# Kernel tuning notes

Hardware: AMD Instinct MI355X
Metric: run time of the kernel (lower is better)

## Reference

```python
import jax, jax.numpy as jnp
import numpy as np

N_NODES = 100000
N_EDGES = 1600000
IN_DIM = 128
EMB = 64
HID = 2 * EMB  # 128


def gcn_conv(x, W, b, row, col, norm):
    # PyG GCNConv: h = x @ W, then aggregate norm-weighted messages src->dst, then +bias
    h = x @ W                                   # [N, out]
    msg = norm[:, None] * h[row]                # gather over source nodes [E', out]
    out = jax.ops.segment_sum(msg, col, num_segments=N_NODES)  # scatter to targets
    return out + b


def gcn_norm(edge_index, edge_weight, n_nodes):
    # add self-loops with weight 1, then symmetric normalization D^-1/2 A D^-1/2
    loop = jnp.arange(n_nodes, dtype=edge_index.dtype)
    row = jnp.concatenate([edge_index[0], loop])
    col = jnp.concatenate([edge_index[1], loop])
    ew = jnp.concatenate([edge_weight, jnp.ones((n_nodes,), edge_weight.dtype)])
    deg = jax.ops.segment_sum(ew, col, num_segments=n_nodes)
    dinv = jnp.where(deg > 0, jax.lax.rsqrt(deg), 0.0)
    norm = dinv[row] * ew * dinv[col]
    return row, col, norm


def setup_inputs() -> dict:
    key = jax.random.key(0)
    ks = jax.random.split(key, 10)
    x = jax.random.normal(ks[0], (N_NODES, IN_DIM), dtype=jnp.float32)
    edge_index = jax.random.randint(ks[1], (2, N_EDGES), 0, N_NODES, dtype=jnp.int64)
    edge_weight = jax.random.uniform(ks[2], (N_EDGES,), dtype=jnp.float32)
    s1 = 1.0 / np.sqrt(IN_DIM)
    s2 = 1.0 / np.sqrt(HID)
    W1 = jax.random.uniform(ks[3], (IN_DIM, HID), jnp.float32, -s1, s1)
    b1 = jnp.zeros((HID,), jnp.float32)
    Wmu = jax.random.uniform(ks[4], (HID, EMB), jnp.float32, -s2, s2)
    bmu = jnp.zeros((EMB,), jnp.float32)
    Wlv = jax.random.uniform(ks[5], (HID, EMB), jnp.float32, -s2, s2)
    blv = jnp.zeros((EMB,), jnp.float32)
    return {"x": x, "edge_index": edge_index, "edge_weight": edge_weight,
            "W1": W1, "b1": b1, "Wmu": Wmu, "bmu": bmu, "Wlv": Wlv, "blv": blv}


def reference(x, edge_index, edge_weight, W1, b1, Wmu, bmu, Wlv, blv):
    row, col, norm = gcn_norm(edge_index, edge_weight, N_NODES)
    h = jax.nn.relu(gcn_conv(x, W1, b1, row, col, norm))
    mu = gcn_conv(h, Wmu, bmu, row, col, norm)
    logvar = gcn_conv(h, Wlv, blv, row, col, norm)
    return (mu, logvar)
```

## Files before the change

kernel.cpp:

```cpp
#include <hip/hip_runtime.h>

#define NN 100000
#define NE 1600000
#define DD 128
#define OUT_HALF 6400000
#define CAP 64

#define NB 256
#define NPB 391
#define BCAP 8192
#define BSTRIDE 64
#define CHUNK 6144
#define CPT 24

#define GNM 64
#define XPITCH 140

typedef unsigned int uint_t;
typedef float v4f __attribute__((ext_vector_type(4)));
typedef short v8s __attribute__((ext_vector_type(8)));

__device__ __forceinline__ unsigned short f2bf(float f) {
    uint_t u = __float_as_uint(f);
    u = (u + 0x7fffu + ((u >> 16) & 1u)) >> 16;
    return (unsigned short)u;
}
__device__ __forceinline__ float bf2f(unsigned short h) {
    return __uint_as_float(((uint_t)h) << 16);
}
__device__ __forceinline__ float bf_lo(uint_t u) { return __uint_as_float(u << 16); }
__device__ __forceinline__ float bf_hi(uint_t u) { return __uint_as_float(u & 0xffff0000u); }

#define EW_SCALE 32767.0f
#define EW_INV (1.0f / 32767.0f)


__global__ void k_zero(int* __restrict__ bcnt) {
    int i = blockIdx.x * blockDim.x + threadIdx.x;
    if (i < NB * BSTRIDE) bcnt[i] = 0;
}

__launch_bounds__(256)
__global__ void k_bin(const int* __restrict__ row, const int* __restrict__ col,
                      const float* __restrict__ ew, int* __restrict__ bcnt,
                      uint2* __restrict__ bins) {
    __shared__ uint2 sorted[CHUNK];
    __shared__ int hist[NB];
    __shared__ int lstart[NB];
    __shared__ int offs[NB];
    __shared__ int gbase[NB];
    const int tid = threadIdx.x;
    const int ebase = blockIdx.x * CHUNK;
    const int nloc = (NE - ebase < CHUNK) ? (NE - ebase) : CHUNK;

    hist[tid] = 0;
    __syncthreads();

    for (int k = 0; k < CPT; ++k) {
        int i = ebase + k * 256 + tid;
        if (i < NE) {
            uint_t b = (uint_t)col[i] / NPB;
            atomicAdd(&hist[b], 1);
        }
    }
    __syncthreads();

    int v = hist[tid];
#pragma unroll
    for (int s = 1; s < NB; s <<= 1) {
        int t = (tid >= s) ? hist[tid - s] : 0;
        __syncthreads();
        hist[tid] += t;
        __syncthreads();
    }
    int excl = hist[tid] - v;
    lstart[tid] = excl;
    offs[tid] = excl;
    gbase[tid] = atomicAdd(&bcnt[tid * BSTRIDE], v);
    __syncthreads();

    for (int k = 0; k < CPT; ++k) {
        int i = ebase + k * 256 + tid;
        if (i < NE) {
            uint_t c = (uint_t)col[i];
            uint_t r = (uint_t)row[i];
            uint_t q = (uint_t)__float2int_rn(ew[i] * EW_SCALE);
            uint_t b = c / NPB;
            int pos = atomicAdd(&offs[b], 1);
            sorted[pos] = make_uint2((r << 15) | q, c);
        }
    }
    __syncthreads();

    for (int i = tid; i < nloc; i += 256) {
        uint2 rec = sorted[i];
        uint_t b = rec.y / NPB;
        int dst = gbase[b] + (i - lstart[b]);
        if (dst < BCAP) bins[(size_t)b * BCAP + dst] = rec;
    }
}

__launch_bounds__(512)
__global__ void k_scatter(const int* __restrict__ bcnt, const uint2* __restrict__ bins,
                          int* __restrict__ cnt, uint_t* __restrict__ slots,
                          float* __restrict__ dinv) {
    __shared__ int combo[NPB];
    const int b = blockIdx.x;
    const int tid = threadIdx.x;
    if (tid < NPB) combo[tid] = 0;
    __syncthreads();
    int n = bcnt[b * BSTRIDE];
    n = (n < BCAP) ? n : BCAP;
    const int base = b * NPB;
    const uint2* seg = bins + (size_t)b * BCAP;
    for (int i = tid; i < n; i += 512) {
        uint2 rec = seg[i];
        int lc = (int)rec.y - base;
        uint_t w = rec.x & 0x7fffu;
        uint_t old = (uint_t)atomicAdd(&combo[lc], (int)((1u << 22) | w));
        uint_t pos = old >> 22;
        if (pos < CAP) slots[rec.y * CAP + pos] = rec.x;
    }
    __syncthreads();
    if (tid < NPB) {
        int node = base + tid;
        if (node < NN) {
            uint_t v = (uint_t)combo[tid];
            int c = (int)(v >> 22);
            cnt[node] = (c < CAP) ? c : CAP;
            dinv[node] = rsqrtf(1.0f + (float)(v & 0x3fffffu) * EW_INV);
        }
    }
}


template <bool RELU, bool OUT_BF16>
__launch_bounds__(256)
__global__ void k_gather(const uint_t* __restrict__ src, const int* __restrict__ cnt,
                         const uint_t* __restrict__ slots, const float* __restrict__ dinv,
                         const float* __restrict__ bias, void* __restrict__ dst) {
    int wid = (blockIdx.x * blockDim.x + threadIdx.x) >> 6;
    int lane = threadIdx.x & 63;
    if (wid >= NN) return;
    float di = dinv[wid];
    uint_t u = src[wid * 64 + lane];
    float accx = bf_lo(u);
    float accy = bf_hi(u);
    int end = __builtin_amdgcn_readfirstlane(cnt[wid]);
    const uint_t* seg = slots + wid * CAP;
    for (int jj = 0; jj < end; jj += 8) {
        uint_t rp[8];
#pragma unroll
        for (int q = 0; q < 8; ++q) {
            int idx = (jj + q < end) ? (jj + q) : (end - 1);
            rp[q] = seg[idx];
        }
        uint_t sv[8];
#pragma unroll
        for (int q = 0; q < 8; ++q) {
            sv[q] = src[(rp[q] >> 15) * 64 + lane];
        }
#pragma unroll
        for (int q = 0; q < 8; ++q) {
            float p = (jj + q < end) ? (float)(rp[q] & 0x7fffu) * EW_INV : 0.0f;
            accx = fmaf(p, bf_lo(sv[q]), accx);
            accy = fmaf(p, bf_hi(sv[q]), accy);
        }
    }
    accx *= di;
    accy *= di;
    if (RELU) {
        float2 b = ((const float2*)bias)[lane];
        accx = fmaxf(accx + b.x, 0.0f) * di;
        accy = fmaxf(accy + b.y, 0.0f) * di;
    }
    if (OUT_BF16) {
        ((uint_t*)dst)[wid * 64 + lane] =
            (uint_t)f2bf(accx) | ((uint_t)f2bf(accy) << 16);
    } else {
        ((float2*)dst)[wid * 64 + lane] = make_float2(accx, accy);
    }
}


__launch_bounds__(256)
__global__ void k_gemm_h0(const float* __restrict__ X, const float* __restrict__ W,
                          const float* __restrict__ dinv,
                          unsigned short* __restrict__ Y) {
    __shared__ float xs[GNM * XPITCH];
    const int tid = threadIdx.x;
    const int node0 = blockIdx.x * GNM;

    {
        const float4* X4 = (const float4*)X;
        for (int i = tid; i < GNM * 32; i += 256) {
            int row = i >> 5, kg = i & 31;
            int ne = node0 + row;
            if (ne >= NN) ne = NN - 1;
            *(float4*)&xs[row * XPITCH + kg * 4] = X4[ne * 32 + kg];
        }
    }
    __syncthreads();

    const int wave = tid >> 6, lane = tid & 63;
    const int la = lane >> 4, ln = lane & 15;
    const float* xrow = &xs[(wave * 16 + ln) * XPITCH];

    v4f acc[8];
#pragma unroll
    for (int nt = 0; nt < 8; ++nt) acc[nt] = (v4f){0.f, 0.f, 0.f, 0.f};

    for (int kt = 0; kt < 4; ++kt) {
        float4 xa0 = *(const float4*)&xrow[kt * 32 + la * 4];
        float4 xa1 = *(const float4*)&xrow[kt * 32 + la * 4 + 16];
        float xv[8] = {xa0.x, xa0.y, xa0.z, xa0.w, xa1.x, xa1.y, xa1.z, xa1.w};
        v8s ah, al;
#pragma unroll
        for (int j = 0; j < 8; ++j) {
            unsigned short h = f2bf(xv[j]);
            ah[j] = (short)h;
            al[j] = (short)f2bf(xv[j] - bf2f(h));
        }
        const float* Wb = W + (kt * 32 + la * 4) * 128 + ln;
#pragma unroll
        for (int nt = 0; nt < 8; ++nt) {
            v8s bh;
#pragma unroll
            for (int j4 = 0; j4 < 4; ++j4) {
                bh[j4] = (short)f2bf(Wb[j4 * 128 + nt * 16]);
                bh[j4 + 4] = (short)f2bf(Wb[(j4 + 16) * 128 + nt * 16]);
            }
            acc[nt] = __builtin_amdgcn_mfma_f32_16x16x32_bf16(ah, bh, acc[nt], 0, 0, 0);
            acc[nt] = __builtin_amdgcn_mfma_f32_16x16x32_bf16(al, bh, acc[nt], 0, 0, 0);
        }
    }

#pragma unroll
    for (int r = 0; r < 4; ++r) {
        int node = node0 + wave * 16 + la * 4 + r;
        if (node < NN) {
            float di = dinv[node];
#pragma unroll
            for (int nt = 0; nt < 8; ++nt)
                Y[node * 128 + nt * 16 + ln] = f2bf(acc[nt][r] * di);
        }
    }
}

__launch_bounds__(256)
__global__ void k_gemm_out(const float* __restrict__ G, const float* __restrict__ Wmu,
                           const float* __restrict__ Wlv, const float* __restrict__ bmu,
                           const float* __restrict__ blv, float* __restrict__ out) {
    __shared__ float xs[GNM * XPITCH];
    const int tid = threadIdx.x;
    const int node0 = blockIdx.x * GNM;

    {
        const float4* G4 = (const float4*)G;
        for (int i = tid; i < GNM * 32; i += 256) {
            int row = i >> 5, kg = i & 31;
            int ne = node0 + row;
            if (ne >= NN) ne = NN - 1;
            *(float4*)&xs[row * XPITCH + kg * 4] = G4[ne * 32 + kg];
        }
    }
    __syncthreads();

    const int wave = tid >> 6, lane = tid & 63;
    const int la = lane >> 4, ln = lane & 15;
    const float* xrow = &xs[(wave * 16 + ln) * XPITCH];

    v4f acc[8];
#pragma unroll
    for (int nt = 0; nt < 8; ++nt) acc[nt] = (v4f){0.f, 0.f, 0.f, 0.f};

    for (int kt = 0; kt < 4; ++kt) {
        float4 xa0 = *(const float4*)&xrow[kt * 32 + la * 4];
        float4 xa1 = *(const float4*)&xrow[kt * 32 + la * 4 + 16];
        float xv[8] = {xa0.x, xa0.y, xa0.z, xa0.w, xa1.x, xa1.y, xa1.z, xa1.w};
        v8s ah, al;
#pragma unroll
        for (int j = 0; j < 8; ++j) {
            unsigned short h = f2bf(xv[j]);
            ah[j] = (short)h;
            al[j] = (short)f2bf(xv[j] - bf2f(h));
        }
        const float* Wmb = Wmu + (kt * 32 + la * 4) * 64 + ln;
        const float* Wlb = Wlv + (kt * 32 + la * 4) * 64 + ln;
#pragma unroll
        for (int nt = 0; nt < 8; ++nt) {
            const float* Wb = (nt < 4) ? Wmb : Wlb;
            const int co = (nt & 3) * 16;
            v8s bh;
#pragma unroll
            for (int j4 = 0; j4 < 4; ++j4) {
                bh[j4] = (short)f2bf(Wb[j4 * 64 + co]);
                bh[j4 + 4] = (short)f2bf(Wb[(j4 + 16) * 64 + co]);
            }
            acc[nt] = __builtin_amdgcn_mfma_f32_16x16x32_bf16(ah, bh, acc[nt], 0, 0, 0);
            acc[nt] = __builtin_amdgcn_mfma_f32_16x16x32_bf16(al, bh, acc[nt], 0, 0, 0);
        }
    }

    float bb[8];
#pragma unroll
    for (int nt = 0; nt < 8; ++nt)
        bb[nt] = (nt < 4) ? bmu[nt * 16 + ln] : blv[(nt - 4) * 16 + ln];

#pragma unroll
    for (int r = 0; r < 4; ++r) {
        int node = node0 + wave * 16 + la * 4 + r;
        if (node < NN) {
#pragma unroll
            for (int nt = 0; nt < 8; ++nt) {
                float v = acc[nt][r] + bb[nt];
                if (nt < 4)
                    out[node * 64 + nt * 16 + ln] = v;
                else
                    out[OUT_HALF + node * 64 + (nt - 4) * 16 + ln] = v;
            }
        }
    }
}


extern "C" void kernel_launch(void* const* d_in, const int* in_sizes, int n_in,
                              void* d_out, int out_size, void* d_ws, size_t ws_size,
                              hipStream_t stream) {
    const float* x   = (const float*)d_in[0];
    const int*   ei  = (const int*)d_in[1];
    const float* ew  = (const float*)d_in[2];
    const float* W1  = (const float*)d_in[3];
    const float* b1  = (const float*)d_in[4];
    const float* Wmu = (const float*)d_in[5];
    const float* bmu = (const float*)d_in[6];
    const float* Wlv = (const float*)d_in[7];
    const float* blv = (const float*)d_in[8];
    const int* rowi = ei;
    const int* coli = ei + NE;
    float* out = (float*)d_out;

    int*    cnt   = (int*)d_ws;
    float*  dinv  = (float*)(cnt + 100352);
    uint_t* slots = (uint_t*)(dinv + 100352);
    float*  poolA = (float*)(slots + NN * CAP);
    unsigned short* y0 = (unsigned short*)poolA;
    float*  g     = poolA;
    uint_t* y1    = (uint_t*)(poolA + NN * DD);
    uint2*  bins  = (uint2*)poolA;
    int*    bcnt  = (int*)(poolA + NB * BCAP * 2);

    const int B = 256;
    const int GGRID = (NN + GNM - 1) / GNM;
    k_zero<<<(NB * BSTRIDE + B - 1) / B, B, 0, stream>>>(bcnt);
    k_bin<<<(NE + CHUNK - 1) / CHUNK, B, 0, stream>>>(rowi, coli, ew, bcnt, bins);
    k_scatter<<<NB, 512, 0, stream>>>(bcnt, bins, cnt, slots, dinv);
    k_gemm_h0<<<GGRID, B, 0, stream>>>(x, W1, dinv, y0);
    k_gather<true, true><<<(NN * 64 + B - 1) / B, B, 0, stream>>>(
        (const uint_t*)y0, cnt, slots, dinv, b1, y1);
    k_gather<false, false><<<(NN * 64 + B - 1) / B, B, 0, stream>>>(
        y1, cnt, slots, dinv, b1, g);
    k_gemm_out<<<GGRID, B, 0, stream>>>(g, Wmu, Wlv, bmu, blv, out);
}
```

Baseline: 349.5 us.

## Split gather aggregation into 8 feature-column tiles with tile-major layout

Reorganizes the bf16 intermediate activations into a tile-major layout of 8 column tiles of 16 features. Each gather block now processes 32 nodes for a single tile, with 8 lanes per node. This is meant to shrink the working set of random source-row gathers so it fits in cache better. The cost is divergent per-node edge loops within a wave and reading the slot lists once per tile.

```diff
diff --git a/kernel.cpp b/kernel.cpp
--- a/kernel.cpp
+++ b/kernel.cpp
@@ -15,6 +15,7 @@
 
 #define GNM 64
 #define XPITCH 140
+
 
 typedef unsigned int uint_t;
 typedef float v4f __attribute__((ext_vector_type(4)));
@@ -139,15 +140,19 @@
 __global__ void k_gather(const uint_t* __restrict__ src, const int* __restrict__ cnt,
                          const uint_t* __restrict__ slots, const float* __restrict__ dinv,
                          const float* __restrict__ bias, void* __restrict__ dst) {
-    int wid = (blockIdx.x * blockDim.x + threadIdx.x) >> 6;
-    int lane = threadIdx.x & 63;
-    if (wid >= NN) return;
-    float di = dinv[wid];
-    uint_t u = src[wid * 64 + lane];
+    const int tile = blockIdx.x & 7;
+    const int nb = blockIdx.x >> 3;
+    const int tid = threadIdx.x;
+    const int node = nb * 32 + (tid >> 3);
+    const int li = tid & 7;
+    const uint_t* srcT = src + (size_t)tile * (NN * 8);
+
+    float di = dinv[node];
+    uint_t u = srcT[node * 8 + li];
     float accx = bf_lo(u);
     float accy = bf_hi(u);
-    int end = __builtin_amdgcn_readfirstlane(cnt[wid]);
-    const uint_t* seg = slots + wid * CAP;
+    int end = cnt[node];
+    const uint_t* seg = slots + node * CAP;
     for (int jj = 0; jj < end; jj += 8) {
         uint_t rp[8];
 #pragma unroll
@@ -158,7 +163,7 @@
         uint_t sv[8];
 #pragma unroll
         for (int q = 0; q < 8; ++q) {
-            sv[q] = src[(rp[q] >> 15) * 64 + lane];
+            sv[q] = srcT[(rp[q] >> 15) * 8 + li];
         }
 #pragma unroll
         for (int q = 0; q < 8; ++q) {
@@ -170,15 +175,15 @@
     accx *= di;
     accy *= di;
     if (RELU) {
-        float2 b = ((const float2*)bias)[lane];
+        float2 b = ((const float2*)bias)[tile * 8 + li];
         accx = fmaxf(accx + b.x, 0.0f) * di;
         accy = fmaxf(accy + b.y, 0.0f) * di;
     }
     if (OUT_BF16) {
-        ((uint_t*)dst)[wid * 64 + lane] =
+        ((uint_t*)dst)[(size_t)tile * (NN * 8) + node * 8 + li] =
             (uint_t)f2bf(accx) | ((uint_t)f2bf(accy) << 16);
     } else {
-        ((float2*)dst)[wid * 64 + lane] = make_float2(accx, accy);
+        ((float2*)dst)[node * 64 + tile * 8 + li] = make_float2(accx, accy);
     }
 }
 
@@ -242,7 +247,7 @@
             float di = dinv[node];
 #pragma unroll
             for (int nt = 0; nt < 8; ++nt)
-                Y[node * 128 + nt * 16 + ln] = f2bf(acc[nt][r] * di);
+                Y[(size_t)nt * (NN * 16) + node * 16 + ln] = f2bf(acc[nt][r] * di);
         }
     }
 }
@@ -352,13 +357,14 @@
 
     const int B = 256;
     const int GGRID = (NN + GNM - 1) / GNM;
+    const int AGGRID = (NN / 32) * 8;
     k_zero<<<(NB * BSTRIDE + B - 1) / B, B, 0, stream>>>(bcnt);
     k_bin<<<(NE + CHUNK - 1) / CHUNK, B, 0, stream>>>(rowi, coli, ew, bcnt, bins);
     k_scatter<<<NB, 512, 0, stream>>>(bcnt, bins, cnt, slots, dinv);
     k_gemm_h0<<<GGRID, B, 0, stream>>>(x, W1, dinv, y0);
-    k_gather<true, true><<<(NN * 64 + B - 1) / B, B, 0, stream>>>(
+    k_gather<true, true><<<AGGRID, B, 0, stream>>>(
         (const uint_t*)y0, cnt, slots, dinv, b1, y1);
-    k_gather<false, false><<<(NN * 64 + B - 1) / B, B, 0, stream>>>(
+    k_gather<false, false><<<AGGRID, B, 0, stream>>>(
         y1, cnt, slots, dinv, b1, g);
     k_gemm_out<<<GGRID, B, 0, stream>>>(g, Wmu, Wlv, bmu, blv, out);
 }
```

Result: slower. 405.1 us (+15.9%).

## Prepack GEMM weights into bf16 MFMA fragments and widen gather unroll to 16

Applied to the files above, without the earlier changes.

Adds two small kernels that convert W1 and Wmu/Wlv into bf16 in the exact per-lane MFMA B-fragment layout. The two GEMMs then load one 16-byte vector per fragment instead of eight strided fp32 loads plus conversions. The gather loop batch also grows from 8 to 16 neighbours per iteration, so more independent loads are in flight. In exchange there are two extra launches and workspace aliasing of the packed weights inside poolA. The wider batch also raises register use and adds wasted padded loads for low-degree nodes.

```diff
diff --git a/kernel.cpp b/kernel.cpp
--- a/kernel.cpp
+++ b/kernel.cpp
@@ -148,20 +148,20 @@
     float accy = bf_hi(u);
     int end = __builtin_amdgcn_readfirstlane(cnt[wid]);
     const uint_t* seg = slots + wid * CAP;
-    for (int jj = 0; jj < end; jj += 8) {
-        uint_t rp[8];
-#pragma unroll
-        for (int q = 0; q < 8; ++q) {
+    for (int jj = 0; jj < end; jj += 16) {
+        uint_t rp[16];
+#pragma unroll
+        for (int q = 0; q < 16; ++q) {
             int idx = (jj + q < end) ? (jj + q) : (end - 1);
             rp[q] = seg[idx];
         }
-        uint_t sv[8];
-#pragma unroll
-        for (int q = 0; q < 8; ++q) {
+        uint_t sv[16];
+#pragma unroll
+        for (int q = 0; q < 16; ++q) {
             sv[q] = src[(rp[q] >> 15) * 64 + lane];
         }
 #pragma unroll
-        for (int q = 0; q < 8; ++q) {
+        for (int q = 0; q < 16; ++q) {
             float p = (jj + q < end) ? (float)(rp[q] & 0x7fffu) * EW_INV : 0.0f;
             accx = fmaf(p, bf_lo(sv[q]), accx);
             accy = fmaf(p, bf_hi(sv[q]), accy);
@@ -183,8 +183,39 @@
 }
 
 
+__global__ void k_wpack1(const float* __restrict__ W, unsigned short* __restrict__ P) {
+    int e = blockIdx.x * blockDim.x + threadIdx.x;
+    if (e >= 2048) return;
+    int ln = e & 15, nt = (e >> 4) & 7, la = (e >> 7) & 3, kt = e >> 9;
+    v8s v;
+#pragma unroll
+    for (int j = 0; j < 8; ++j) {
+        int k = kt * 32 + la * 4 + (j & 3) + 16 * (j >> 2);
+        v[j] = (short)f2bf(W[k * 128 + nt * 16 + ln]);
+    }
+    *(v8s*)&P[e * 8] = v;
+}
+
+__global__ void k_wpack2(const float* __restrict__ Wmu, const float* __restrict__ Wlv,
+                         unsigned short* __restrict__ P) {
+    int e = blockIdx.x * blockDim.x + threadIdx.x;
+    if (e >= 2048) return;
+    int ln = e & 15, nt = (e >> 4) & 7, la = (e >> 7) & 3, kt = e >> 9;
+    v8s v;
+#pragma unroll
+    for (int j = 0; j < 8; ++j) {
+        int k = kt * 32 + la * 4 + (j & 3) + 16 * (j >> 2);
+        float f = (nt < 4) ? Wmu[k * 64 + nt * 16 + ln]
+                           : Wlv[k * 64 + (nt - 4) * 16 + ln];
+        v[j] = (short)f2bf(f);
+    }
+    *(v8s*)&P[e * 8] = v;
+}
+
+
 __launch_bounds__(256)
-__global__ void k_gemm_h0(const float* __restrict__ X, const float* __restrict__ W,
+__global__ void k_gemm_h0(const float* __restrict__ X,
+                          const unsigned short* __restrict__ Wpk,
                           const float* __restrict__ dinv,
                           unsigned short* __restrict__ Y) {
     __shared__ float xs[GNM * XPITCH];
@@ -205,6 +236,7 @@
     const int wave = tid >> 6, lane = tid & 63;
     const int la = lane >> 4, ln = lane & 15;
     const float* xrow = &xs[(wave * 16 + ln) * XPITCH];
+    const v8s* Wf = (const v8s*)Wpk;
 
     v4f acc[8];
 #pragma unroll
@@ -221,15 +253,10 @@
             ah[j] = (short)h;
             al[j] = (short)f2bf(xv[j] - bf2f(h));
         }
-        const float* Wb = W + (kt * 32 + la * 4) * 128 + ln;
+        const int wbase = (kt * 4 + la) * 8 * 16;
 #pragma unroll
         for (int nt = 0; nt < 8; ++nt) {
-            v8s bh;
-#pragma unroll
-            for (int j4 = 0; j4 < 4; ++j4) {
-                bh[j4] = (short)f2bf(Wb[j4 * 128 + nt * 16]);
-                bh[j4 + 4] = (short)f2bf(Wb[(j4 + 16) * 128 + nt * 16]);
-            }
+            v8s bh = Wf[wbase + nt * 16 + ln];
             acc[nt] = __builtin_amdgcn_mfma_f32_16x16x32_bf16(ah, bh, acc[nt], 0, 0, 0);
             acc[nt] = __builtin_amdgcn_mfma_f32_16x16x32_bf16(al, bh, acc[nt], 0, 0, 0);
         }
@@ -248,9 +275,10 @@
 }
 
 __launch_bounds__(256)
-__global__ void k_gemm_out(const float* __restrict__ G, const float* __restrict__ Wmu,
-                           const float* __restrict__ Wlv, const float* __restrict__ bmu,
-                           const float* __restrict__ blv, float* __restrict__ out) {
+__global__ void k_gemm_out(const float* __restrict__ G,
+                           const unsigned short* __restrict__ Wpk,
+                           const float* __restrict__ bmu, const float* __restrict__ blv,
+                           float* __restrict__ out) {
     __shared__ float xs[GNM * XPITCH];
     const int tid = threadIdx.x;
     const int node0 = blockIdx.x * GNM;
@@ -269,6 +297,7 @@
     const int wave = tid >> 6, lane = tid & 63;
     const int la = lane >> 4, ln = lane & 15;
     const float* xrow = &xs[(wave * 16 + ln) * XPITCH];
+    const v8s* Wf = (const v8s*)Wpk;
 
     v4f acc[8];
 #pragma unroll
@@ -285,18 +314,10 @@
             ah[j] = (short)h;
             al[j] = (short)f2bf(xv[j] - bf2f(h));
         }
-        const float* Wmb = Wmu + (kt * 32 + la * 4) * 64 + ln;
-        const float* Wlb = Wlv + (kt * 32 + la * 4) * 64 + ln;
+        const int wbase = (kt * 4 + la) * 8 * 16;
 #pragma unroll
         for (int nt = 0; nt < 8; ++nt) {
-            const float* Wb = (nt < 4) ? Wmb : Wlb;
-            const int co = (nt & 3) * 16;
-            v8s bh;
-#pragma unroll
-            for (int j4 = 0; j4 < 4; ++j4) {
-                bh[j4] = (short)f2bf(Wb[j4 * 64 + co]);
-                bh[j4 + 4] = (short)f2bf(Wb[(j4 + 16) * 64 + co]);
-            }
+            v8s bh = Wf[wbase + nt * 16 + ln];
             acc[nt] = __builtin_amdgcn_mfma_f32_16x16x32_bf16(ah, bh, acc[nt], 0, 0, 0);
             acc[nt] = __builtin_amdgcn_mfma_f32_16x16x32_bf16(al, bh, acc[nt], 0, 0, 0);
         }
@@ -344,21 +365,25 @@
     float*  dinv  = (float*)(cnt + 100352);
     uint_t* slots = (uint_t*)(dinv + 100352);
     float*  poolA = (float*)(slots + NN * CAP);
-    unsigned short* y0 = (unsigned short*)poolA;
+    uint_t* y0    = (uint_t*)poolA;
     float*  g     = poolA;
     uint_t* y1    = (uint_t*)(poolA + NN * DD);
     uint2*  bins  = (uint2*)poolA;
     int*    bcnt  = (int*)(poolA + NB * BCAP * 2);
+    unsigned short* Wpk1 = (unsigned short*)(poolA + NN * 64);
+    unsigned short* Wpk2 = (unsigned short*)(poolA + NN * DD);
 
     const int B = 256;
     const int GGRID = (NN + GNM - 1) / GNM;
     k_zero<<<(NB * BSTRIDE + B - 1) / B, B, 0, stream>>>(bcnt);
     k_bin<<<(NE + CHUNK - 1) / CHUNK, B, 0, stream>>>(rowi, coli, ew, bcnt, bins);
     k_scatter<<<NB, 512, 0, stream>>>(bcnt, bins, cnt, slots, dinv);
-    k_gemm_h0<<<GGRID, B, 0, stream>>>(x, W1, dinv, y0);
+    k_wpack1<<<8, B, 0, stream>>>(W1, Wpk1);
+    k_gemm_h0<<<GGRID, B, 0, stream>>>(x, Wpk1, dinv, (unsigned short*)y0);
     k_gather<true, true><<<(NN * 64 + B - 1) / B, B, 0, stream>>>(
-        (const uint_t*)y0, cnt, slots, dinv, b1, y1);
+        y0, cnt, slots, dinv, b1, y1);
     k_gather<false, false><<<(NN * 64 + B - 1) / B, B, 0, stream>>>(
         y1, cnt, slots, dinv, b1, g);
-    k_gemm_out<<<GGRID, B, 0, stream>>>(g, Wmu, Wlv, bmu, blv, out);
-}
+    k_wpack2<<<8, B, 0, stream>>>(Wmu, Wlv, Wpk2);
+    k_gemm_out<<<GGRID, B, 0, stream>>>(g, Wpk2, bmu, blv, out);
+}
```

Measured after the change: 324.9 us. 7.0% less time.
